# Kernel tuning notes

Hardware: AMD Instinct MI355X
Metric: run time of the kernel (lower is better)

## Reference

```python
import jax, jax.numpy as jnp
import numpy as np

N_NODES = 50000


def gcn_conv(x, edge_index, W, b):
    """PyG GCNConv: add self-loops, symmetric deg^{-1/2} norm, W then aggregate."""
    n = x.shape[0]
    loops = jnp.arange(n, dtype=edge_index.dtype)
    src = jnp.concatenate([edge_index[0], loops])  # message sources
    dst = jnp.concatenate([edge_index[1], loops])  # aggregation targets
    h = x @ W  # [N, out_dim] -- transform before gather (PyG order)
    deg = jax.ops.segment_sum(jnp.ones_like(dst, dtype=h.dtype), dst, num_segments=n)
    dinv = jnp.where(deg > 0, jax.lax.rsqrt(jnp.maximum(deg, 1.0)), 0.0)
    norm = dinv[src] * dinv[dst]  # [E+N]
    msg = h[src] * norm[:, None]  # gather + normalize
    out = jax.ops.segment_sum(msg, dst, num_segments=n)  # scatter-add
    return out + b


def setup_inputs() -> dict:
    key = jax.random.key(0)
    k1, k2, k3, k4, k5 = jax.random.split(key, 5)
    N, E, D_IN, D_H, D_OUT = N_NODES, 800000, 128, 256, 16
    x = jax.random.normal(k1, (N, D_IN), dtype=jnp.float32)
    edge_index = jax.random.randint(k2, (2, E), 0, N, dtype=jnp.int64)
    s1 = 1.0 / np.sqrt(D_IN)
    s2 = 1.0 / np.sqrt(D_H)
    W1 = jax.random.uniform(k3, (D_IN, D_H), jnp.float32, -s1, s1)
    b1 = jnp.zeros((D_H,), jnp.float32)
    W2 = jax.random.uniform(k4, (D_H, D_OUT), jnp.float32, -s2, s2)
    b2 = jnp.zeros((D_OUT,), jnp.float32)
    return {"x": x, "edge_index": edge_index, "W1": W1, "b1": b1, "W2": W2, "b2": b2}


def reference(x, edge_index, W1, b1, W2, b2):
    h = jax.nn.relu(gcn_conv(x, edge_index, W1, b1))
    # dropout is identity in eval mode
    logits = gcn_conv(h, edge_index, W2, b2)
    return jax.nn.log_softmax(logits, axis=-1)
```

## Files before the change

kernel.cpp:

```cpp
#include <hip/hip_runtime.h>
#include <math.h>

typedef unsigned int uint;
typedef short short8 __attribute__((ext_vector_type(8)));
typedef float floatx4 __attribute__((ext_vector_type(4)));

union U4S8 { uint4 u; short8 s; };

#define CAP 64


__device__ __forceinline__ float blo(uint u) { return __uint_as_float(u << 16); }
__device__ __forceinline__ float bhi(uint u) { return __uint_as_float(u & 0xffff0000u); }
__device__ __forceinline__ uint pack_bf16(float a, float b) {
    uint ua = __float_as_uint(a), ub = __float_as_uint(b);
    ua = (ua + 0x7fffu + ((ua >> 16) & 1u)) >> 16;
    ub = (ub + 0x7fffu + ((ub >> 16) & 1u)) >> 16;
    return ua | (ub << 16);
}
__device__ __forceinline__ unsigned short rb16(float f) {
    uint u = __float_as_uint(f);
    return (unsigned short)((u + 0x7fffu + ((u >> 16) & 1u)) >> 16);
}


__global__ void k_init(int* __restrict__ cnt, int n,
                       const float* __restrict__ W1, const float* __restrict__ W2,
                       uint* __restrict__ W1t, uint* __restrict__ W2t) {
    int i = blockIdx.x * 256 + threadIdx.x;
    if (i < n) cnt[i] = 0;
    if (i < 16384) {
        int nn = i >> 6, kd = i & 63;
        W1t[i] = pack_bf16(W1[(size_t)(2 * kd) * 256 + nn], W1[(size_t)(2 * kd + 1) * 256 + nn]);
    } else if (i < 16384 + 2048) {
        int j = i - 16384;
        int o = j >> 7, kd = j & 127;
        W2t[j] = pack_bf16(W2[(size_t)(2 * kd) * 16 + o], W2[(size_t)(2 * kd + 1) * 16 + o]);
    }
}


__global__ void k_bucket(const int* __restrict__ ei, int E,
                         int* __restrict__ cnt, int* __restrict__ colb) {
    int e = blockIdx.x * 256 + threadIdx.x;
    if (e >= E) return;
    int s = ei[e], t = ei[E + e];
    int slot = atomicAdd(cnt + t, 1);
    if (slot < CAP) colb[(t << 6) + slot] = s;
}


__global__ void k_dinv_cast(const int* __restrict__ cnt, const float2* __restrict__ x2,
                            float* __restrict__ dinv, uint* __restrict__ xsb, int total) {
    int j = blockIdx.x * 256 + threadIdx.x;
    if (j >= total) return;
    int row = j >> 6, lane = j & 63;
    float di = rsqrtf((float)cnt[row] + 1.0f);
    if (lane == 0) dinv[row] = di;
    float2 v = x2[j];
    xsb[j] = pack_bf16(v.x * di, v.y * di);
}


__global__ __launch_bounds__(256) void k_agg_csr128(
    const int* __restrict__ cnt, const int* __restrict__ colb,
    const float* __restrict__ dinv, const uint* __restrict__ xsb,
    uint* __restrict__ outb, int n)
{
    int node = (blockIdx.x * 256 + threadIdx.x) >> 6;
    int lane = threadIdx.x & 63;
    if (node >= n) return;
    float di = dinv[node];
    int deg = min(cnt[node], CAP);
    const int* bucket = colb + (node << 6);
    uint u = xsb[(size_t)node * 64 + lane];
    float ax = blo(u), ay = bhi(u);
    int j = 0;
    for (; j + 8 <= deg; j += 8) {
        int s0 = bucket[j],     s1 = bucket[j + 1], s2 = bucket[j + 2], s3 = bucket[j + 3];
        int s4 = bucket[j + 4], s5 = bucket[j + 5], s6 = bucket[j + 6], s7 = bucket[j + 7];
        uint u0 = xsb[(size_t)s0 * 64 + lane];
        uint u1 = xsb[(size_t)s1 * 64 + lane];
        uint u2 = xsb[(size_t)s2 * 64 + lane];
        uint u3 = xsb[(size_t)s3 * 64 + lane];
        uint u4 = xsb[(size_t)s4 * 64 + lane];
        uint u5 = xsb[(size_t)s5 * 64 + lane];
        uint u6 = xsb[(size_t)s6 * 64 + lane];
        uint u7 = xsb[(size_t)s7 * 64 + lane];
        ax += blo(u0) + blo(u1) + blo(u2) + blo(u3) + blo(u4) + blo(u5) + blo(u6) + blo(u7);
        ay += bhi(u0) + bhi(u1) + bhi(u2) + bhi(u3) + bhi(u4) + bhi(u5) + bhi(u6) + bhi(u7);
    }
    for (; j < deg; ++j) {
        uint uu = xsb[(size_t)bucket[j] * 64 + lane];
        ax += blo(uu); ay += bhi(uu);
    }
    outb[(size_t)node * 64 + lane] = pack_bf16(ax * di, ay * di);
}


__global__ __launch_bounds__(256) void k_gemm_mfma(
    const uint* __restrict__ Ab,
    const uint* __restrict__ W1t,
    const float* __restrict__ b1,
    const uint* __restrict__ W2t,
    const float* __restrict__ dinv,
    float* __restrict__ H2, int M)
{
    __shared__ uint Alds[64 * 68];
    __shared__ uint Hlds[64 * 132];

    const int t    = threadIdx.x;
    const int mb   = blockIdx.x * 64;
    const int wv   = t >> 6;
    const int lane = t & 63;
    const int c    = lane & 15;
    const int q    = lane >> 4;

    #pragma unroll
    for (int it = 0; it < 4; ++it) {
        int i = it * 256 + t;
        int r = i >> 4, cc = i & 15;
        int gr = mb + r;
        uint4 v = make_uint4(0u, 0u, 0u, 0u);
        if (gr < M) v = ((const uint4*)Ab)[(size_t)gr * 16 + cc];
        *(uint4*)&Alds[r * 68 + cc * 4] = v;
    }
    __syncthreads();

    floatx4 acc[4][4];
    #pragma unroll
    for (int i = 0; i < 4; ++i)
        #pragma unroll
        for (int jj = 0; jj < 4; ++jj) acc[i][jj] = (floatx4)0.f;

    #pragma unroll
    for (int kk = 0; kk < 4; ++kk) {
        U4S8 af[4];
        #pragma unroll
        for (int mt = 0; mt < 4; ++mt)
            af[mt].u = *(const uint4*)&Alds[(mt * 16 + c) * 68 + kk * 16 + q * 4];
        #pragma unroll
        for (int nt = 0; nt < 4; ++nt) {
            int n = wv * 64 + nt * 16 + c;
            U4S8 bf;
            bf.u = ((const uint4*)W1t)[(size_t)n * 16 + kk * 4 + q];
            #pragma unroll
            for (int mt = 0; mt < 4; ++mt)
                acc[mt][nt] = __builtin_amdgcn_mfma_f32_16x16x32_bf16(
                    af[mt].s, bf.s, acc[mt][nt], 0, 0, 0);
        }
    }

    float b1v[4];
    #pragma unroll
    for (int nt = 0; nt < 4; ++nt) b1v[nt] = b1[wv * 64 + nt * 16 + c];

    unsigned short* hs = (unsigned short*)Hlds;
    #pragma unroll
    for (int mt = 0; mt < 4; ++mt)
        #pragma unroll
        for (int nt = 0; nt < 4; ++nt)
            #pragma unroll
            for (int r = 0; r < 4; ++r) {
                float hv = fmaxf(acc[mt][nt][r] + b1v[nt], 0.f);
                int row = mt * 16 + q * 4 + r;
                int colc = wv * 64 + nt * 16 + c;
                hs[row * 264 + colc] = rb16(hv);
            }
    __syncthreads();

    floatx4 acc2 = (floatx4)0.f;
    #pragma unroll
    for (int kk = 0; kk < 8; ++kk) {
        U4S8 av, bv;
        av.u = *(const uint4*)&Hlds[(wv * 16 + c) * 132 + kk * 16 + q * 4];
        bv.u = ((const uint4*)W2t)[(size_t)c * 32 + kk * 4 + q];
        acc2 = __builtin_amdgcn_mfma_f32_16x16x32_bf16(av.s, bv.s, acc2, 0, 0, 0);
    }
    #pragma unroll
    for (int r = 0; r < 4; ++r) {
        int gr = mb + wv * 16 + q * 4 + r;
        if (gr < M) H2[(size_t)gr * 16 + c] = acc2[r] * dinv[gr];
    }
}


__global__ __launch_bounds__(256) void k_agg_csr16_lsm(
    const int* __restrict__ cnt, const int* __restrict__ colb,
    const float* __restrict__ dinv, const float* __restrict__ h2s,
    const float* __restrict__ b2, float* __restrict__ out, int n)
{
    int node = (blockIdx.x * 256 + threadIdx.x) >> 4;
    int lane = threadIdx.x & 15;
    if (node >= n) return;
    float di = dinv[node];
    int deg = min(cnt[node], CAP);
    const int* bucket = colb + (node << 6);
    float acc = h2s[(size_t)node * 16 + lane];
    int j = 0;
    for (; j + 8 <= deg; j += 8) {
        int s0 = bucket[j],     s1 = bucket[j + 1], s2 = bucket[j + 2], s3 = bucket[j + 3];
        int s4 = bucket[j + 4], s5 = bucket[j + 5], s6 = bucket[j + 6], s7 = bucket[j + 7];
        float v0 = h2s[(size_t)s0 * 16 + lane];
        float v1 = h2s[(size_t)s1 * 16 + lane];
        float v2 = h2s[(size_t)s2 * 16 + lane];
        float v3 = h2s[(size_t)s3 * 16 + lane];
        float v4 = h2s[(size_t)s4 * 16 + lane];
        float v5 = h2s[(size_t)s5 * 16 + lane];
        float v6 = h2s[(size_t)s6 * 16 + lane];
        float v7 = h2s[(size_t)s7 * 16 + lane];
        acc += v0 + v1 + v2 + v3 + v4 + v5 + v6 + v7;
    }
    for (; j < deg; ++j) acc += h2s[(size_t)bucket[j] * 16 + lane];
    acc = acc * di + b2[lane];
    float m = acc;
    #pragma unroll
    for (int msk = 1; msk < 16; msk <<= 1) m = fmaxf(m, __shfl_xor(m, msk, 16));
    float ex = __expf(acc - m);
    float ssum = ex;
    #pragma unroll
    for (int msk = 1; msk < 16; msk <<= 1) ssum += __shfl_xor(ssum, msk, 16);
    out[(size_t)node * 16 + lane] = acc - m - __logf(ssum);
}


extern "C" void kernel_launch(void* const* d_in, const int* in_sizes, int n_in,
                              void* d_out, int out_size, void* d_ws, size_t ws_size,
                              hipStream_t stream) {
    const float* x  = (const float*)d_in[0];
    const int*   ei = (const int*)d_in[1];
    const float* W1 = (const float*)d_in[2];
    const float* b1 = (const float*)d_in[3];
    const float* W2 = (const float*)d_in[4];
    const float* b2 = (const float*)d_in[5];
    float* out = (float*)d_out;

    const int N = in_sizes[0] / 128;
    const int E = in_sizes[1] / 2;

    float* ws    = (float*)d_ws;
    float* dinv  = ws;
    int*   cnt   = (int*)(ws + 51200);
    int*   colb  = (int*)(ws + 102400);
    uint*  xsb   = (uint*)(ws + 3302400);
    uint*  aggb  = (uint*)(ws + 6502400);
    float* h2s   = ws + 9702400;
    uint*  W1t   = (uint*)(ws + 10502400);
    uint*  W2t   = (uint*)(ws + 10518784);

    const int NB = (N + 255) / 256;

    k_init     <<<NB, 256, 0, stream>>>(cnt, N, W1, W2, W1t, W2t);
    k_bucket   <<<(E + 255) / 256, 256, 0, stream>>>(ei, E, cnt, colb);
    k_dinv_cast<<<(N * 64 + 255) / 256, 256, 0, stream>>>(cnt, (const float2*)x, dinv, xsb, N * 64);

    k_agg_csr128<<<(N * 64 + 255) / 256, 256, 0, stream>>>(cnt, colb, dinv, xsb, aggb, N);
    k_gemm_mfma <<<(N + 63) / 64, 256, 0, stream>>>(aggb, W1t, b1, W2t, dinv, h2s, N);
    k_agg_csr16_lsm<<<(N * 16 + 255) / 256, 256, 0, stream>>>(cnt, colb, dinv, h2s, b2, out, N);
}
```

Before: 204.4 us.

## Fuse bucketing, bf16 cast and weight packing; compute dinv on the fly

Merges edge bucketing, the x-to-bf16 cast and the W1/W2 repacking into one launch, and replaces the init kernel with hipMemsetAsync. The dinv array is dropped, so the cast no longer waits on degree counts. Each consumer instead recomputes rsqrt from cnt, and the layer-1 aggregation scales every gathered neighbour by its own dinv. This removes a launch and a pass over x, at the cost of an extra scattered cnt load and an rsqrt per edge in the aggregation. It also adds nontemporal stores for the bucket writes.

```diff
diff --git a/kernel.cpp b/kernel.cpp
--- a/kernel.cpp
+++ b/kernel.cpp
@@ -23,78 +23,84 @@
     return (unsigned short)((u + 0x7fffu + ((u >> 16) & 1u)) >> 16);
 }
 
-
-__global__ void k_init(int* __restrict__ cnt, int n,
-                       const float* __restrict__ W1, const float* __restrict__ W2,
-                       uint* __restrict__ W1t, uint* __restrict__ W2t) {
+__device__ __forceinline__ float dinv_of(int c) { return rsqrtf((float)c + 1.0f); }
+
+
+__global__ void k_bucket_cast(const int* __restrict__ ei, int E, int castN,
+                              int* __restrict__ cnt, int* __restrict__ colb,
+                              const float4* __restrict__ x4, uint2* __restrict__ xb2,
+                              const float* __restrict__ W1, const float* __restrict__ W2,
+                              uint* __restrict__ W1t, uint* __restrict__ W2t) {
     int i = blockIdx.x * 256 + threadIdx.x;
-    if (i < n) cnt[i] = 0;
-    if (i < 16384) {
-        int nn = i >> 6, kd = i & 63;
-        W1t[i] = pack_bf16(W1[(size_t)(2 * kd) * 256 + nn], W1[(size_t)(2 * kd + 1) * 256 + nn]);
-    } else if (i < 16384 + 2048) {
-        int j = i - 16384;
-        int o = j >> 7, kd = j & 127;
-        W2t[j] = pack_bf16(W2[(size_t)(2 * kd) * 16 + o], W2[(size_t)(2 * kd + 1) * 16 + o]);
-    }
-}
-
-
-__global__ void k_bucket(const int* __restrict__ ei, int E,
-                         int* __restrict__ cnt, int* __restrict__ colb) {
-    int e = blockIdx.x * 256 + threadIdx.x;
-    if (e >= E) return;
-    int s = ei[e], t = ei[E + e];
-    int slot = atomicAdd(cnt + t, 1);
-    if (slot < CAP) colb[(t << 6) + slot] = s;
-}
-
-
-__global__ void k_dinv_cast(const int* __restrict__ cnt, const float2* __restrict__ x2,
-                            float* __restrict__ dinv, uint* __restrict__ xsb, int total) {
-    int j = blockIdx.x * 256 + threadIdx.x;
-    if (j >= total) return;
-    int row = j >> 6, lane = j & 63;
-    float di = rsqrtf((float)cnt[row] + 1.0f);
-    if (lane == 0) dinv[row] = di;
-    float2 v = x2[j];
-    xsb[j] = pack_bf16(v.x * di, v.y * di);
-}
-
-
-__global__ __launch_bounds__(256) void k_agg_csr128(
+    if (i < E) {
+        int s = ei[i], t = ei[E + i];
+        int slot = atomicAdd(cnt + t, 1);
+        if (slot < CAP)
+            __builtin_nontemporal_store(s, colb + (t << 6) + slot);
+    } else if (i < E + castN) {
+        int j = i - E;
+        float4 v = x4[j];
+        uint2 o;
+        o.x = pack_bf16(v.x, v.y);
+        o.y = pack_bf16(v.z, v.w);
+        xb2[j] = o;
+    } else {
+        int j = i - E - castN;
+        if (j < 16384) {
+            int nn = j >> 6, kd = j & 63;
+            W1t[j] = pack_bf16(W1[(size_t)(2 * kd) * 256 + nn],
+                               W1[(size_t)(2 * kd + 1) * 256 + nn]);
+        } else if (j < 18432) {
+            int jj = j - 16384;
+            int o = jj >> 7, kd = jj & 127;
+            W2t[jj] = pack_bf16(W2[(size_t)(2 * kd) * 16 + o],
+                                W2[(size_t)(2 * kd + 1) * 16 + o]);
+        }
+    }
+}
+
+
+__global__ __launch_bounds__(256) void k_agg128(
     const int* __restrict__ cnt, const int* __restrict__ colb,
-    const float* __restrict__ dinv, const uint* __restrict__ xsb,
-    uint* __restrict__ outb, int n)
+    const uint* __restrict__ xb, uint* __restrict__ aggb, int n)
 {
     int node = (blockIdx.x * 256 + threadIdx.x) >> 6;
     int lane = threadIdx.x & 63;
     if (node >= n) return;
-    float di = dinv[node];
-    int deg = min(cnt[node], CAP);
+    int degf = cnt[node];
+    float di = dinv_of(degf);
+    int deg = min(degf, CAP);
     const int* bucket = colb + (node << 6);
-    uint u = xsb[(size_t)node * 64 + lane];
-    float ax = blo(u), ay = bhi(u);
+    uint u = xb[(size_t)node * 64 + lane];
+    float ax = blo(u) * di, ay = bhi(u) * di;
     int j = 0;
     for (; j + 8 <= deg; j += 8) {
-        int s0 = bucket[j],     s1 = bucket[j + 1], s2 = bucket[j + 2], s3 = bucket[j + 3];
+        int s0 = bucket[j + 0], s1 = bucket[j + 1], s2 = bucket[j + 2], s3 = bucket[j + 3];
         int s4 = bucket[j + 4], s5 = bucket[j + 5], s6 = bucket[j + 6], s7 = bucket[j + 7];
-        uint u0 = xsb[(size_t)s0 * 64 + lane];
-        uint u1 = xsb[(size_t)s1 * 64 + lane];
-        uint u2 = xsb[(size_t)s2 * 64 + lane];
-        uint u3 = xsb[(size_t)s3 * 64 + lane];
-        uint u4 = xsb[(size_t)s4 * 64 + lane];
-        uint u5 = xsb[(size_t)s5 * 64 + lane];
-        uint u6 = xsb[(size_t)s6 * 64 + lane];
-        uint u7 = xsb[(size_t)s7 * 64 + lane];
-        ax += blo(u0) + blo(u1) + blo(u2) + blo(u3) + blo(u4) + blo(u5) + blo(u6) + blo(u7);
-        ay += bhi(u0) + bhi(u1) + bhi(u2) + bhi(u3) + bhi(u4) + bhi(u5) + bhi(u6) + bhi(u7);
+        float d0 = dinv_of(cnt[s0]), d1 = dinv_of(cnt[s1]);
+        float d2 = dinv_of(cnt[s2]), d3 = dinv_of(cnt[s3]);
+        float d4 = dinv_of(cnt[s4]), d5 = dinv_of(cnt[s5]);
+        float d6 = dinv_of(cnt[s6]), d7 = dinv_of(cnt[s7]);
+        uint u0 = xb[(size_t)s0 * 64 + lane];
+        uint u1 = xb[(size_t)s1 * 64 + lane];
+        uint u2 = xb[(size_t)s2 * 64 + lane];
+        uint u3 = xb[(size_t)s3 * 64 + lane];
+        uint u4 = xb[(size_t)s4 * 64 + lane];
+        uint u5 = xb[(size_t)s5 * 64 + lane];
+        uint u6 = xb[(size_t)s6 * 64 + lane];
+        uint u7 = xb[(size_t)s7 * 64 + lane];
+        ax += blo(u0) * d0 + blo(u1) * d1 + blo(u2) * d2 + blo(u3) * d3
+            + blo(u4) * d4 + blo(u5) * d5 + blo(u6) * d6 + blo(u7) * d7;
+        ay += bhi(u0) * d0 + bhi(u1) * d1 + bhi(u2) * d2 + bhi(u3) * d3
+            + bhi(u4) * d4 + bhi(u5) * d5 + bhi(u6) * d6 + bhi(u7) * d7;
     }
     for (; j < deg; ++j) {
-        uint uu = xsb[(size_t)bucket[j] * 64 + lane];
-        ax += blo(uu); ay += bhi(uu);
-    }
-    outb[(size_t)node * 64 + lane] = pack_bf16(ax * di, ay * di);
+        int s = bucket[j];
+        float d = dinv_of(cnt[s]);
+        uint uu = xb[(size_t)s * 64 + lane];
+        ax += blo(uu) * d; ay += bhi(uu) * d;
+    }
+    aggb[(size_t)node * 64 + lane] = pack_bf16(ax * di, ay * di);
 }
 
 
@@ -103,7 +109,7 @@
     const uint* __restrict__ W1t,
     const float* __restrict__ b1,
     const uint* __restrict__ W2t,
-    const float* __restrict__ dinv,
+    const int* __restrict__ cnt,
     float* __restrict__ H2, int M)
 {
     __shared__ uint Alds[64 * 68];
@@ -180,21 +186,22 @@
     #pragma unroll
     for (int r = 0; r < 4; ++r) {
         int gr = mb + wv * 16 + q * 4 + r;
-        if (gr < M) H2[(size_t)gr * 16 + c] = acc2[r] * dinv[gr];
-    }
-}
-
-
-__global__ __launch_bounds__(256) void k_agg_csr16_lsm(
+        if (gr < M) H2[(size_t)gr * 16 + c] = acc2[r] * dinv_of(cnt[gr]);
+    }
+}
+
+
+__global__ __launch_bounds__(256) void k_agg16_lsm(
     const int* __restrict__ cnt, const int* __restrict__ colb,
-    const float* __restrict__ dinv, const float* __restrict__ h2s,
-    const float* __restrict__ b2, float* __restrict__ out, int n)
+    const float* __restrict__ h2s, const float* __restrict__ b2,
+    float* __restrict__ out, int n)
 {
     int node = (blockIdx.x * 256 + threadIdx.x) >> 4;
     int lane = threadIdx.x & 15;
     if (node >= n) return;
-    float di = dinv[node];
-    int deg = min(cnt[node], CAP);
+    int degf = cnt[node];
+    float di = dinv_of(degf);
+    int deg = min(degf, CAP);
     const int* bucket = colb + (node << 6);
     float acc = h2s[(size_t)node * 16 + lane];
     int j = 0;
@@ -235,26 +242,30 @@
     const float* b2 = (const float*)d_in[5];
     float* out = (float*)d_out;
 
-    const int N = in_sizes[0] / 128;
-    const int E = in_sizes[1] / 2;
+    int N = in_sizes[0] / 128;
+    int E = in_sizes[1] / 2;
 
     float* ws    = (float*)d_ws;
-    float* dinv  = ws;
-    int*   cnt   = (int*)(ws + 51200);
-    int*   colb  = (int*)(ws + 102400);
-    uint*  xsb   = (uint*)(ws + 3302400);
-    uint*  aggb  = (uint*)(ws + 6502400);
-    float* h2s   = ws + 9702400;
-    uint*  W1t   = (uint*)(ws + 10502400);
-    uint*  W2t   = (uint*)(ws + 10518784);
-
-    const int NB = (N + 255) / 256;
-
-    k_init     <<<NB, 256, 0, stream>>>(cnt, N, W1, W2, W1t, W2t);
-    k_bucket   <<<(E + 255) / 256, 256, 0, stream>>>(ei, E, cnt, colb);
-    k_dinv_cast<<<(N * 64 + 255) / 256, 256, 0, stream>>>(cnt, (const float2*)x, dinv, xsb, N * 64);
-
-    k_agg_csr128<<<(N * 64 + 255) / 256, 256, 0, stream>>>(cnt, colb, dinv, xsb, aggb, N);
-    k_gemm_mfma <<<(N + 63) / 64, 256, 0, stream>>>(aggb, W1t, b1, W2t, dinv, h2s, N);
-    k_agg_csr16_lsm<<<(N * 16 + 255) / 256, 256, 0, stream>>>(cnt, colb, dinv, h2s, b2, out, N);
-}
+    int*   cnt   = (int*)ws;
+    int*   colb  = (int*)(ws + 51200);
+    uint*  xb    = (uint*)(ws + 3251200);
+    uint*  aggb  = (uint*)(ws + 6451200);
+    float* h2s   = ws + 9651200;
+    uint*  W1t   = (uint*)(ws + 10451200);
+    uint*  W2t   = (uint*)(ws + 10467584);
+
+    hipMemsetAsync(cnt, 0, (size_t)N * sizeof(int), stream);
+
+    {
+        int castN = N * 32;
+        int tot = E + castN + 18432;
+        k_bucket_cast<<<(tot + 255) / 256, 256, 0, stream>>>(
+            ei, E, castN, cnt, colb, (const float4*)x, (uint2*)xb, W1, W2, W1t, W2t);
+    }
+
+    k_agg128<<<(N * 64 + 255) / 256, 256, 0, stream>>>(cnt, colb, xb, aggb, N);
+
+    k_gemm_mfma<<<(N + 63) / 64, 256, 0, stream>>>(aggb, W1t, b1, W2t, cnt, h2s, N);
+
+    k_agg16_lsm<<<(N * 16 + 255) / 256, 256, 0, stream>>>(cnt, colb, h2s, b2, out, N);
+}
```

After: 204.5 us. About the same (+0.0%).
